# Kernel tuning notes

Measured on AMD Instinct MI355X. Metric: run time of the kernel, lower is better.

The kernel has to match this reference:

```python
import jax, jax.numpy as jnp
import numpy as np

IN_FEATURES = 4096
OUT_FEATURES = 11008
TOKENS = 2048  # batch*seq flattened


def setup_inputs() -> dict:
    key = jax.random.key(0)
    k_x, k_w, k_s, k_z, k_b = jax.random.split(key, 5)
    x = jax.random.normal(k_x, (TOKENS, IN_FEATURES), dtype=jnp.float32)
    qweight = jax.random.randint(k_w, (OUT_FEATURES, IN_FEATURES), 0, 256, dtype=jnp.int32).astype(jnp.uint8)
    # realistic small positive scales, zero points in mid-range
    scale = jax.random.uniform(k_s, (OUT_FEATURES, 1), dtype=jnp.float32, minval=0.001, maxval=0.02)
    zero_point = jax.random.uniform(k_z, (OUT_FEATURES, 1), dtype=jnp.float32, minval=0.0, maxval=255.0)
    bias = jax.random.normal(k_b, (OUT_FEATURES,), dtype=jnp.float32)
    return {"x": x, "qweight": qweight, "scale": scale, "zero_point": zero_point, "bias": bias}


def reference(x, qweight, scale, zero_point, bias) -> jnp.ndarray:
    # dequantize: (q - zp) * s, per output channel  -> [out, in]
    w = (qweight.astype(scale.dtype) - zero_point) * scale
    # F.linear: x @ w.T + bias -> [tokens, out]
    return jnp.einsum("ti,oi->to", x, w) + bias
```

## Files before the change

### kernel.cpp

```cpp
#include <hip/hip_runtime.h>
#include <hip/hip_bf16.h>
#include <stdint.h>

typedef __bf16 bf16_t;
typedef bf16_t bf16x8 __attribute__((ext_vector_type(8)));
typedef float  f32x4  __attribute__((ext_vector_type(4)));
typedef int    i32x4  __attribute__((ext_vector_type(4)));

#define M_TOK 2048
#define N_OUT 11008
#define K_IN  4096
#define N16   (N_OUT / 16)
#define NTILE 688

__global__ __launch_bounds__(256)
void prep(const int* __restrict__ Q, const float* __restrict__ X,
          signed char* __restrict__ W8t, signed char* __restrict__ X8t,
          float* __restrict__ dxv, float* __restrict__ sxv)
{
    __shared__ float wmax[4];
    __shared__ int   wsum[4];
    const int tid = threadIdx.x;

    if (blockIdx.x < N16) {
        const int n16 = blockIdx.x;
        const int fr  = tid & 15;
        const int fg  = (tid >> 4) & 3;
        const int w   = tid >> 6;
        const int* qrow = Q + (size_t)(n16 * 16 + fr) * K_IN + fg * 16;
        signed char* wout = W8t + ((size_t)n16 * 64 + (tid & 63)) * 16;
        #pragma unroll 4
        for (int kt2 = 0; kt2 < 16; ++kt2) {
            const int kt = kt2 * 4 + w;
            const int4* q4 = (const int4*)(qrow + kt * 64);
            unsigned int pk[4];
            #pragma unroll
            for (int j = 0; j < 4; ++j) {
                const int4 q = q4[j];
                pk[j] =  (unsigned int)((q.x - 128) & 255)
                      | ((unsigned int)((q.y - 128) & 255) << 8)
                      | ((unsigned int)((q.z - 128) & 255) << 16)
                      | ((unsigned int)((q.w - 128) & 255) << 24);
            }
            *(int4*)(wout + (size_t)kt * (N16 * 1024)) = *(const int4*)pk;
        }
        return;
    }

    const int row = blockIdx.x - N16;
    const float* xr = X + (size_t)row * K_IN + tid * 16;
    float v[16];
    #pragma unroll
    for (int j = 0; j < 4; ++j)
        *(float4*)(v + j * 4) = ((const float4*)xr)[j];

    float amax = 0.f;
    #pragma unroll
    for (int j = 0; j < 16; ++j) amax = fmaxf(amax, fabsf(v[j]));
    #pragma unroll
    for (int m = 1; m < 64; m <<= 1)
        amax = fmaxf(amax, __shfl_xor(amax, m));
    const int wv = tid >> 6;
    if ((tid & 63) == 0) wmax[wv] = amax;
    __syncthreads();
    amax = fmaxf(fmaxf(wmax[0], wmax[1]), fmaxf(wmax[2], wmax[3]));
    amax = fmaxf(amax, 1e-20f);
    const float inv = 127.f / amax;

    int sum = 0;
    unsigned int pk[4];
    #pragma unroll
    for (int j = 0; j < 4; ++j) {
        unsigned int p = 0;
        #pragma unroll
        for (int i = 0; i < 4; ++i) {
            int xi = (int)__builtin_rintf(v[j * 4 + i] * inv);
            xi = max(-127, min(127, xi));
            sum += xi;
            p |= ((unsigned int)(xi & 255)) << (8 * i);
        }
        pk[j] = p;
    }
    const size_t toff = (((size_t)(tid >> 2) * 128 + (row >> 4)) * 64
                         + (size_t)((tid & 3) * 16 + (row & 15))) * 16;
    *(int4*)(X8t + toff) = *(const int4*)pk;

    #pragma unroll
    for (int m = 1; m < 64; m <<= 1) sum += __shfl_xor(sum, m);
    if ((tid & 63) == 0) wsum[wv] = sum;
    __syncthreads();
    if (tid == 0) {
        dxv[row] = amax * (1.f / 127.f);
        sxv[row] = (float)(wsum[0] + wsum[1] + wsum[2] + wsum[3]);
    }
}


#define LOAD_A4B4(DA, DB, KT) do {                                             \
    const char* ap_ = gAt + (size_t)(KT) * (128 * 1024);                       \
    DA##0 = *(const i32x4*)(ap_ + 0 * 1024);                                   \
    DA##1 = *(const i32x4*)(ap_ + 1 * 1024);                                   \
    DA##2 = *(const i32x4*)(ap_ + 2 * 1024);                                   \
    DA##3 = *(const i32x4*)(ap_ + 3 * 1024);                                   \
    const char* bp_ = gBt + (size_t)(KT) * (N16 * 1024);                       \
    DB##0 = *(const i32x4*)(bp_ + 0 * 1024);                                   \
    DB##1 = *(const i32x4*)(bp_ + 1 * 1024);                                   \
    DB##2 = *(const i32x4*)(bp_ + 2 * 1024);                                   \
    DB##3 = *(const i32x4*)(bp_ + 3 * 1024);                                   \
} while (0)

#define LOAD_B4(DB, KT) do {                                                   \
    const char* bp_ = gBt + (size_t)(KT) * (N16 * 1024);                       \
    DB##4 = *(const i32x4*)(bp_ + 4 * 1024);                                   \
    DB##5 = *(const i32x4*)(bp_ + 5 * 1024);                                   \
    DB##6 = *(const i32x4*)(bp_ + 6 * 1024);                                   \
    DB##7 = *(const i32x4*)(bp_ + 7 * 1024);                                   \
} while (0)

#define MMQ(FA, FB, MQ, NQ)                                                    \
    acc[MQ][NQ] = __builtin_amdgcn_mfma_i32_16x16x64_i8(FA##MQ, FB##NQ, acc[MQ][NQ], 0, 0, 0)

#define MFMA16_LO(FA, FB) do {                                                 \
    __builtin_amdgcn_s_setprio(1);                                             \
    MMQ(FA, FB, 0, 0); MMQ(FA, FB, 0, 1); MMQ(FA, FB, 0, 2); MMQ(FA, FB, 0, 3);\
    MMQ(FA, FB, 0, 4); MMQ(FA, FB, 0, 5); MMQ(FA, FB, 0, 6); MMQ(FA, FB, 0, 7);\
    MMQ(FA, FB, 1, 0); MMQ(FA, FB, 1, 1); MMQ(FA, FB, 1, 2); MMQ(FA, FB, 1, 3);\
    MMQ(FA, FB, 1, 4); MMQ(FA, FB, 1, 5); MMQ(FA, FB, 1, 6); MMQ(FA, FB, 1, 7);\
    __builtin_amdgcn_s_setprio(0);                                             \
} while (0)

#define MFMA16_HI(FA, FB) do {                                                 \
    __builtin_amdgcn_s_setprio(1);                                             \
    MMQ(FA, FB, 2, 0); MMQ(FA, FB, 2, 1); MMQ(FA, FB, 2, 2); MMQ(FA, FB, 2, 3);\
    MMQ(FA, FB, 2, 4); MMQ(FA, FB, 2, 5); MMQ(FA, FB, 2, 6); MMQ(FA, FB, 2, 7);\
    MMQ(FA, FB, 3, 0); MMQ(FA, FB, 3, 1); MMQ(FA, FB, 3, 2); MMQ(FA, FB, 3, 3);\
    MMQ(FA, FB, 3, 4); MMQ(FA, FB, 3, 5); MMQ(FA, FB, 3, 6); MMQ(FA, FB, 3, 7);\
    __builtin_amdgcn_s_setprio(0);                                             \
} while (0)

#define REGION14(CA, CB, NA, NB, KTN) do {                                     \
    LOAD_A4B4(NA, NB, KTN);                                                    \
    MFMA16_LO(CA, CB);                                                         \
    LOAD_B4(NB, KTN);                                                          \
    MFMA16_HI(CA, CB);                                                         \
} while (0)

__global__ __launch_bounds__(256, 2)
void gemm_i8(const signed char* __restrict__ A8t,
             const signed char* __restrict__ B8t,
             const float* __restrict__ dxv,
             const float* __restrict__ sxv,
             const float* __restrict__ S,
             const float* __restrict__ Z,
             const float* __restrict__ Bias,
             float* __restrict__ O)
{
    const int tid  = threadIdx.x;
    const int lane = tid & 63;
    const int wid  = tid >> 6;
    const int wr   = wid >> 1;
    const int wc   = wid & 1;
    const int fr   = lane & 15;
    const int fg   = lane >> 4;

    const int bid = blockIdx.x;
    const int xcd = bid & 7;
    const int k   = bid >> 3;
    int col, by;
    if (k < 80) { col = 5 * xcd + (k >> 4); by = k & 15; }
    else        { const int e = k - 80; col = 40 + (e >> 1); by = 2 * xcd + (e & 1); }
    const long bm = (long)by * 128;
    const long bn = (long)col * 256;

    const char* gAt = (const char*)A8t
                    + (((size_t)(by * 8 + wr * 4)) * 64 + lane) * 16;
    const char* gBt = (const char*)B8t
                    + (((size_t)(col * 16 + wc * 8)) * 64 + lane) * 16;

    i32x4 acc[4][8] = {};
    i32x4 pa0, pa1, pa2, pa3, pb0, pb1, pb2, pb3, pb4, pb5, pb6, pb7;
    i32x4 qa0, qa1, qa2, qa3, qb0, qb1, qb2, qb3, qb4, qb5, qb6, qb7;

    LOAD_A4B4(pa, pb, 0);
    LOAD_B4(pb, 0);

    #pragma unroll 1
    for (int i = 0; i < 31; ++i) {
        REGION14(pa, pb, qa, qb, 2 * i + 1);
        REGION14(qa, qb, pa, pb, 2 * i + 2);
    }
    REGION14(pa, pb, qa, qb, 63);
    MFMA16_LO(qa, qb);
    MFMA16_HI(qa, qb);

    float dxa[16], sxa[16];
    #pragma unroll
    for (int m = 0; m < 4; ++m)
        #pragma unroll
        for (int r = 0; r < 4; ++r) {
            const int row = (int)bm + wr * 64 + m * 16 + (fg << 2) + r;
            dxa[m * 4 + r] = dxv[row];
            sxa[m * 4 + r] = sxv[row];
        }
    #pragma unroll
    for (int n = 0; n < 8; ++n) {
        const long ocol = bn + wc * 128 + n * 16 + fr;
        const float s  = S[ocol];
        const float f  = 128.f - Z[ocol];
        const float bi = Bias[ocol];
        #pragma unroll
        for (int m = 0; m < 4; ++m) {
            const long row0 = bm + wr * 64 + m * 16 + (fg << 2);
            #pragma unroll
            for (int r = 0; r < 4; ++r) {
                const float g = (float)acc[m][n][r] + f * sxa[m * 4 + r];
                O[(size_t)(row0 + r) * N_OUT + ocol] = s * dxa[m * 4 + r] * g + bi;
            }
        }
    }
}

__global__ __launch_bounds__(256)
void qlinear_fused(const float* __restrict__ X,
                   const int*   __restrict__ Q,
                   const float* __restrict__ S,
                   const float* __restrict__ Z,
                   const float* __restrict__ Bias,
                   float* __restrict__ O)
{
    __shared__ bf16_t As[128][32];
    __shared__ bf16_t Bs[128][32];
    const int tid = threadIdx.x, lane = tid & 63, wid = tid >> 6;
    const int wr = wid >> 1, wc = wid & 1, fr = lane & 15, fg = lane >> 4;
    const int bm = blockIdx.y * 128, bn = blockIdx.x * 128;
    const int srow = tid >> 1, scol = (tid & 1) << 4;
    const float s_n = S[bn + srow];
    const float zs_n = Z[bn + srow] * s_n;
    const float* xptr = X + (size_t)(bm + srow) * K_IN + scol;
    const int*   qptr = Q + (size_t)(bn + srow) * K_IN + scol;
    f32x4 acc[4][4] = {};
    for (int k0 = 0; k0 < K_IN; k0 += 32) {
        float a[16]; int qi[16];
        { const float4* s4 = (const float4*)(xptr + k0);
          *(float4*)(a+0)=s4[0]; *(float4*)(a+4)=s4[1]; *(float4*)(a+8)=s4[2]; *(float4*)(a+12)=s4[3]; }
        { const int4* s4 = (const int4*)(qptr + k0);
          *(int4*)(qi+0)=s4[0]; *(int4*)(qi+4)=s4[1]; *(int4*)(qi+8)=s4[2]; *(int4*)(qi+12)=s4[3]; }
        float b[16];
        #pragma unroll
        for (int j = 0; j < 16; ++j) b[j] = (float)qi[j] * s_n - zs_n;
        bf16x8 pa0, pa1, pb0, pb1;
        #pragma unroll
        for (int j = 0; j < 8; ++j) {
            pa0[j]=(bf16_t)a[j]; pa1[j]=(bf16_t)a[j+8];
            pb0[j]=(bf16_t)b[j]; pb1[j]=(bf16_t)b[j+8];
        }
        *(bf16x8*)&As[srow][scol]   = pa0; *(bf16x8*)&As[srow][scol+8] = pa1;
        *(bf16x8*)&Bs[srow][scol]   = pb0; *(bf16x8*)&Bs[srow][scol+8] = pb1;
        __syncthreads();
        bf16x8 af[4], bfv[4];
        #pragma unroll
        for (int m = 0; m < 4; ++m) af[m] = *(const bf16x8*)&As[wr*64+m*16+fr][fg*8];
        #pragma unroll
        for (int n = 0; n < 4; ++n) bfv[n] = *(const bf16x8*)&Bs[wc*64+n*16+fr][fg*8];
        #pragma unroll
        for (int m = 0; m < 4; ++m)
            #pragma unroll
            for (int n = 0; n < 4; ++n)
                acc[m][n] = __builtin_amdgcn_mfma_f32_16x16x32_bf16(af[m], bfv[n], acc[m][n], 0,0,0);
        __syncthreads();
    }
    #pragma unroll
    for (int n = 0; n < 4; ++n) {
        const int col = bn + wc*64 + n*16 + fr;
        const float bv = Bias[col];
        #pragma unroll
        for (int m = 0; m < 4; ++m) {
            const int row0 = bm + wr*64 + m*16 + fg*4;
            #pragma unroll
            for (int r = 0; r < 4; ++r)
                O[(size_t)(row0 + r) * N_OUT + col] = acc[m][n][r] + bv;
        }
    }
}

extern "C" void kernel_launch(void* const* d_in, const int* in_sizes, int n_in,
                              void* d_out, int out_size, void* d_ws, size_t ws_size,
                              hipStream_t stream) {
    const float* X    = (const float*)d_in[0];
    const int*   Q    = (const int*)d_in[1];
    const float* S    = (const float*)d_in[2];
    const float* Z    = (const float*)d_in[3];
    const float* Bias = (const float*)d_in[4];
    float* O = (float*)d_out;

    const size_t wbytes = (size_t)N_OUT * K_IN;
    const size_t xbytes = (size_t)M_TOK * K_IN;
    const size_t need   = wbytes + xbytes + 2 * M_TOK * sizeof(float) + 256;

    if (ws_size >= need) {
        signed char* W8t = (signed char*)d_ws;
        signed char* X8t = (signed char*)d_ws + wbytes;
        float* dxv = (float*)((char*)d_ws + wbytes + xbytes);
        float* sxv = dxv + M_TOK;
        prep<<<dim3(N16 + M_TOK), 256, 0, stream>>>(Q, X, W8t, X8t, dxv, sxv);
        gemm_i8<<<dim3(NTILE), 256, 0, stream>>>(X8t, W8t, dxv, sxv, S, Z, Bias, O);
    } else {
        dim3 grid(N_OUT / 128, M_TOK / 128);
        qlinear_fused<<<grid, 256, 0, stream>>>(X, Q, S, Z, Bias, O);
    }
}
```

Before: 171.0 us.

## Halve GEMM block N-tile to 128 and double the tile count

Shrinks the int8 GEMM block tile from 128x256 to 128x128, so each wave holds a 4x4 accumulator grid instead of 4x8. The tile count doubles to 1376 and the XCD-aware block-to-tile mapping is rewritten to match. Loads are issued together before a single 16-MFMA group, and the occupancy hint of 2 is dropped from launch bounds. This cuts register pressure and improves load balance across CUs, but halves arithmetic intensity per loaded A fragment, raising global traffic for A.

```diff
diff --git a/kernel.cpp b/kernel.cpp
--- a/kernel.cpp
+++ b/kernel.cpp
@@ -11,7 +11,7 @@
 #define N_OUT 11008
 #define K_IN  4096
 #define N16   (N_OUT / 16)
-#define NTILE 688
+#define NTILE 1376
 
 __global__ __launch_bounds__(256)
 void prep(const int* __restrict__ Q, const float* __restrict__ X,
@@ -96,12 +96,15 @@
 }
 
 
-#define LOAD_A4B4(DA, DB, KT) do {                                             \
+#define LOAD_A4(DA, KT) do {                                                   \
     const char* ap_ = gAt + (size_t)(KT) * (128 * 1024);                       \
     DA##0 = *(const i32x4*)(ap_ + 0 * 1024);                                   \
     DA##1 = *(const i32x4*)(ap_ + 1 * 1024);                                   \
     DA##2 = *(const i32x4*)(ap_ + 2 * 1024);                                   \
     DA##3 = *(const i32x4*)(ap_ + 3 * 1024);                                   \
+} while (0)
+
+#define LOAD_B4(DB, KT) do {                                                   \
     const char* bp_ = gBt + (size_t)(KT) * (N16 * 1024);                       \
     DB##0 = *(const i32x4*)(bp_ + 0 * 1024);                                   \
     DB##1 = *(const i32x4*)(bp_ + 1 * 1024);                                   \
@@ -109,43 +112,25 @@
     DB##3 = *(const i32x4*)(bp_ + 3 * 1024);                                   \
 } while (0)
 
-#define LOAD_B4(DB, KT) do {                                                   \
-    const char* bp_ = gBt + (size_t)(KT) * (N16 * 1024);                       \
-    DB##4 = *(const i32x4*)(bp_ + 4 * 1024);                                   \
-    DB##5 = *(const i32x4*)(bp_ + 5 * 1024);                                   \
-    DB##6 = *(const i32x4*)(bp_ + 6 * 1024);                                   \
-    DB##7 = *(const i32x4*)(bp_ + 7 * 1024);                                   \
-} while (0)
-
 #define MMQ(FA, FB, MQ, NQ)                                                    \
     acc[MQ][NQ] = __builtin_amdgcn_mfma_i32_16x16x64_i8(FA##MQ, FB##NQ, acc[MQ][NQ], 0, 0, 0)
 
-#define MFMA16_LO(FA, FB) do {                                                 \
+#define MFMA16(FA, FB) do {                                                    \
     __builtin_amdgcn_s_setprio(1);                                             \
     MMQ(FA, FB, 0, 0); MMQ(FA, FB, 0, 1); MMQ(FA, FB, 0, 2); MMQ(FA, FB, 0, 3);\
-    MMQ(FA, FB, 0, 4); MMQ(FA, FB, 0, 5); MMQ(FA, FB, 0, 6); MMQ(FA, FB, 0, 7);\
     MMQ(FA, FB, 1, 0); MMQ(FA, FB, 1, 1); MMQ(FA, FB, 1, 2); MMQ(FA, FB, 1, 3);\
-    MMQ(FA, FB, 1, 4); MMQ(FA, FB, 1, 5); MMQ(FA, FB, 1, 6); MMQ(FA, FB, 1, 7);\
+    MMQ(FA, FB, 2, 0); MMQ(FA, FB, 2, 1); MMQ(FA, FB, 2, 2); MMQ(FA, FB, 2, 3);\
+    MMQ(FA, FB, 3, 0); MMQ(FA, FB, 3, 1); MMQ(FA, FB, 3, 2); MMQ(FA, FB, 3, 3);\
     __builtin_amdgcn_s_setprio(0);                                             \
 } while (0)
 
-#define MFMA16_HI(FA, FB) do {                                                 \
-    __builtin_amdgcn_s_setprio(1);                                             \
-    MMQ(FA, FB, 2, 0); MMQ(FA, FB, 2, 1); MMQ(FA, FB, 2, 2); MMQ(FA, FB, 2, 3);\
-    MMQ(FA, FB, 2, 4); MMQ(FA, FB, 2, 5); MMQ(FA, FB, 2, 6); MMQ(FA, FB, 2, 7);\
-    MMQ(FA, FB, 3, 0); MMQ(FA, FB, 3, 1); MMQ(FA, FB, 3, 2); MMQ(FA, FB, 3, 3);\
-    MMQ(FA, FB, 3, 4); MMQ(FA, FB, 3, 5); MMQ(FA, FB, 3, 6); MMQ(FA, FB, 3, 7);\
-    __builtin_amdgcn_s_setprio(0);                                             \
-} while (0)
-
-#define REGION14(CA, CB, NA, NB, KTN) do {                                     \
-    LOAD_A4B4(NA, NB, KTN);                                                    \
-    MFMA16_LO(CA, CB);                                                         \
+#define REGION17(CA, CB, NA, NB, KTN) do {                                     \
+    LOAD_A4(NA, KTN);                                                          \
     LOAD_B4(NB, KTN);                                                          \
-    MFMA16_HI(CA, CB);                                                         \
-} while (0)
-
-__global__ __launch_bounds__(256, 2)
+    MFMA16(CA, CB);                                                            \
+} while (0)
+
+__global__ __launch_bounds__(256)
 void gemm_i8(const signed char* __restrict__ A8t,
              const signed char* __restrict__ B8t,
              const float* __restrict__ dxv,
@@ -167,31 +152,30 @@
     const int xcd = bid & 7;
     const int k   = bid >> 3;
     int col, by;
-    if (k < 80) { col = 5 * xcd + (k >> 4); by = k & 15; }
-    else        { const int e = k - 80; col = 40 + (e >> 1); by = 2 * xcd + (e & 1); }
+    if (k < 160) { col = 10 * xcd + (k >> 4); by = k & 15; }
+    else         { const int g = xcd * 12 + (k - 160); col = 80 + (g >> 4); by = g & 15; }
     const long bm = (long)by * 128;
-    const long bn = (long)col * 256;
+    const long bn = (long)col * 128;
 
     const char* gAt = (const char*)A8t
                     + (((size_t)(by * 8 + wr * 4)) * 64 + lane) * 16;
     const char* gBt = (const char*)B8t
-                    + (((size_t)(col * 16 + wc * 8)) * 64 + lane) * 16;
-
-    i32x4 acc[4][8] = {};
-    i32x4 pa0, pa1, pa2, pa3, pb0, pb1, pb2, pb3, pb4, pb5, pb6, pb7;
-    i32x4 qa0, qa1, qa2, qa3, qb0, qb1, qb2, qb3, qb4, qb5, qb6, qb7;
-
-    LOAD_A4B4(pa, pb, 0);
+                    + (((size_t)(col * 8 + wc * 4)) * 64 + lane) * 16;
+
+    i32x4 acc[4][4] = {};
+    i32x4 pa0, pa1, pa2, pa3, pb0, pb1, pb2, pb3;
+    i32x4 qa0, qa1, qa2, qa3, qb0, qb1, qb2, qb3;
+
+    LOAD_A4(pa, 0);
     LOAD_B4(pb, 0);
 
     #pragma unroll 1
     for (int i = 0; i < 31; ++i) {
-        REGION14(pa, pb, qa, qb, 2 * i + 1);
-        REGION14(qa, qb, pa, pb, 2 * i + 2);
-    }
-    REGION14(pa, pb, qa, qb, 63);
-    MFMA16_LO(qa, qb);
-    MFMA16_HI(qa, qb);
+        REGION17(pa, pb, qa, qb, 2 * i + 1);
+        REGION17(qa, qb, pa, pb, 2 * i + 2);
+    }
+    REGION17(pa, pb, qa, qb, 63);
+    MFMA16(qa, qb);
 
     float dxa[16], sxa[16];
     #pragma unroll
@@ -203,8 +187,8 @@
             sxa[m * 4 + r] = sxv[row];
         }
     #pragma unroll
-    for (int n = 0; n < 8; ++n) {
-        const long ocol = bn + wc * 128 + n * 16 + fr;
+    for (int n = 0; n < 4; ++n) {
+        const long ocol = bn + wc * 64 + n * 16 + fr;
         const float s  = S[ocol];
         const float f  = 128.f - Z[ocol];
         const float bi = Bias[ocol];
```

Result: slower. 193.1 us (+12.9%).
